# Kernel tuning notes

Hardware: AMD Instinct MI355X
Metric: run time of the kernel (lower is better)

The kernel has to match this reference:

```python
import jax, jax.numpy as jnp
import numpy as np

N = 100000
E = 3200000
C = 32

def setup_inputs() -> dict:
    key = jax.random.key(0)
    k1, k2, k3, k4 = jax.random.split(key, 4)
    adj = jax.random.uniform(k1, (E,), dtype=jnp.float32)          # per-edge weights
    labels = jax.random.uniform(k2, (N, C), dtype=jnp.float32)     # node label distributions
    src = jax.random.randint(k3, (E,), 0, N, dtype=jnp.int64)
    dst = jax.random.randint(k4, (E,), 0, N, dtype=jnp.int64)
    return {"adj": adj, "labels": labels, "src": src, "dst": dst, "n_lpa": 3}

def reference(adj, labels, src, dst, n_lpa):
    # One hop of label propagation: msg_e = label[src_e] * w_e; out_v = sum_{e: dst_e=v} msg_e
    n_nodes = labels.shape[0]

    def lp(lab):
        msg = lab[src] * adj[:, None]                 # [E, C] gather-multiply
        return jax.ops.segment_sum(msg, dst, num_segments=n_nodes)  # scatter-sum over dst

    # soft_label == 0 path of the original forward: plain iterated propagation
    for _ in range(n_lpa):
        labels = lp(labels)
    return labels
```

## Files before the change

kernel.cpp:

```cpp
#include <hip/hip_runtime.h>
#include <hip/hip_bf16.h>


#define LPA_C   32
#define BKT_LG  7
#define BKT_NV  (1 << BKT_LG)
#define CHUNK   6400

__global__ __launch_bounds__(512)
void k_histA(const int* __restrict__ dst, int* __restrict__ C,
             int E, int P, int nbkt) {
    __shared__ int h[1024];
    int c = blockIdx.x;
    int base = c * CHUNK;
    int lim = min(CHUNK, E - base);
    for (int i = threadIdx.x; i < nbkt; i += 512) h[i] = 0;
    __syncthreads();
    for (int i = threadIdx.x; i < lim; i += 512)
        atomicAdd(&h[dst[base + i] >> BKT_LG], 1);
    __syncthreads();
    for (int i = threadIdx.x; i < nbkt; i += 512) C[i * P + c] = h[i];
}

__global__ __launch_bounds__(512)
void k_scanC(int* __restrict__ C, int* __restrict__ btot, int P) {
    __shared__ int s[512];
    int b = blockIdx.x;
    int t = threadIdx.x;
    int v = (t < P) ? C[b * P + t] : 0;
    s[t] = v;
    __syncthreads();
    for (int off = 1; off < 512; off <<= 1) {
        int x = (t >= off) ? s[t - off] : 0;
        __syncthreads();
        s[t] += x;
        __syncthreads();
    }
    if (t < P) C[b * P + t] = s[t] - v;
    if (t == 511) btot[b] = s[511];
}

__global__ __launch_bounds__(1024)
void k_scanB(const int* __restrict__ btot, int* __restrict__ bstart,
             int* __restrict__ row_start, int nb, int N, int E) {
    __shared__ int s[1024];
    int t = threadIdx.x;
    int v = (t < nb) ? btot[t] : 0;
    s[t] = v;
    __syncthreads();
    for (int off = 1; off < 1024; off <<= 1) {
        int x = (t >= off) ? s[t - off] : 0;
        __syncthreads();
        s[t] += x;
        __syncthreads();
    }
    if (t < nb) bstart[t] = s[t] - v;
    if (t == 0) { bstart[nb] = E; row_start[N] = E; }
}

__global__ __launch_bounds__(512)
void k_scatA(const int* __restrict__ src, const int* __restrict__ dst,
             const float* __restrict__ adj, const int* __restrict__ C,
             const int* __restrict__ bstart, int2* __restrict__ mid,
             int E, int P, int nbkt) {
    __shared__ int2 sedge[CHUNK];
    __shared__ int  lofs[1025];
    __shared__ int  cur[1024];
    __shared__ int  s2[512];
    int c = blockIdx.x;
    int base = c * CHUNK;
    int lim = min(CHUNK, E - base);
    int t = threadIdx.x;

    for (int i = t; i < nbkt; i += 512) cur[i] = 0;
    __syncthreads();
    for (int i = t; i < lim; i += 512)
        atomicAdd(&cur[dst[base + i] >> BKT_LG], 1);
    __syncthreads();

    int k0 = 2 * t, k1 = 2 * t + 1;
    int a0 = (k0 < nbkt) ? cur[k0] : 0;
    int a1 = (k1 < nbkt) ? cur[k1] : 0;
    int ts = a0 + a1;
    s2[t] = ts;
    __syncthreads();
    for (int off = 1; off < 512; off <<= 1) {
        int x = (t >= off) ? s2[t - off] : 0;
        __syncthreads();
        s2[t] += x;
        __syncthreads();
    }
    int pre = s2[t] - ts;
    if (k0 < nbkt) lofs[k0] = pre;
    if (k1 < nbkt) lofs[k1] = pre + a0;
    if (t == 0) lofs[nbkt] = lim;
    __syncthreads();
    for (int i = t; i < nbkt; i += 512) cur[i] = lofs[i];
    __syncthreads();

    for (int i = t; i < lim; i += 512) {
        int d = dst[base + i];
        int b = d >> BKT_LG;
        int pos = atomicAdd(&cur[b], 1);
        sedge[pos] = make_int2(src[base + i] | ((d & (BKT_NV - 1)) << 20),
                               __float_as_int(adj[base + i]));
    }
    __syncthreads();

    for (int i = t; i < lim; i += 512) {
        int lo = 0, hi = nbkt;
        while (hi - lo > 1) {
            int m = (lo + hi) >> 1;
            if (lofs[m] <= i) lo = m; else hi = m;
        }
        int gdst = bstart[lo] + C[lo * P + c] + (i - lofs[lo]);
        mid[gdst] = sedge[i];
    }
}

__global__ __launch_bounds__(512)
void k_sortnode(const int2* __restrict__ mid, const int* __restrict__ bstart,
                int2* __restrict__ edges, int* __restrict__ row_start, int N) {
    __shared__ int lcnt[BKT_NV];
    __shared__ int lofs[BKT_NV];
    int b = blockIdx.x;
    int s0 = bstart[b], e0 = bstart[b + 1];
    int v0 = b << BKT_LG;
    int nv = min(BKT_NV, N - v0);

    if (threadIdx.x < BKT_NV) lcnt[threadIdx.x] = 0;
    __syncthreads();
    for (int i = s0 + threadIdx.x; i < e0; i += 512)
        atomicAdd(&lcnt[mid[i].x >> 20], 1);
    __syncthreads();
    if (threadIdx.x < BKT_NV) lofs[threadIdx.x] = lcnt[threadIdx.x];
    __syncthreads();
    for (int off = 1; off < BKT_NV; off <<= 1) {
        int x = 0;
        if (threadIdx.x < BKT_NV && threadIdx.x >= off) x = lofs[threadIdx.x - off];
        __syncthreads();
        if (threadIdx.x < BKT_NV) lofs[threadIdx.x] += x;
        __syncthreads();
    }
    if (threadIdx.x < BKT_NV) {
        int base = s0 + lofs[threadIdx.x] - lcnt[threadIdx.x];
        lcnt[threadIdx.x] = base;
        if (threadIdx.x < nv) row_start[v0 + threadIdx.x] = base;
    }
    __syncthreads();
    for (int i = s0 + threadIdx.x; i < e0; i += 512) {
        int2 ed = mid[i];
        int pos = atomicAdd(&lcnt[ed.x >> 20], 1);
        edges[pos] = make_int2(ed.x & 0xFFFFF, ed.y);
    }
}

__global__ void k_tobf16(const float* __restrict__ in, ushort* __restrict__ out, int n) {
    int i = blockIdx.x * blockDim.x + threadIdx.x;
    if (i < n) out[i] = __bfloat16_as_ushort(__float2bfloat16(in[i]));
}

template <int OUT16>
__global__ void lpa_pull16(const int2* __restrict__ edges,
                           const int* __restrict__ row_start,
                           const ushort* __restrict__ lab_in,
                           void* __restrict__ out_v, int N) {
    int node = blockIdx.x * 8 + (threadIdx.x >> 5);
    int c = threadIdx.x & 31;
    if (node >= N) return;
    int j = row_start[node];
    int end = row_start[node + 1];
    float acc0 = 0.f, acc1 = 0.f;
#define GATH(S) (__uint_as_float((unsigned)lab_in[((size_t)(unsigned)(S) << 5) + c] << 16))
    for (; j + 8 <= end; j += 8) {
        int4 q0 = *(const int4*)(edges + j);
        int4 q1 = *(const int4*)(edges + j + 2);
        int4 q2 = *(const int4*)(edges + j + 4);
        int4 q3 = *(const int4*)(edges + j + 6);
        acc0 += __int_as_float(q0.y) * GATH(q0.x);
        acc1 += __int_as_float(q0.w) * GATH(q0.z);
        acc0 += __int_as_float(q1.y) * GATH(q1.x);
        acc1 += __int_as_float(q1.w) * GATH(q1.z);
        acc0 += __int_as_float(q2.y) * GATH(q2.x);
        acc1 += __int_as_float(q2.w) * GATH(q2.z);
        acc0 += __int_as_float(q3.y) * GATH(q3.x);
        acc1 += __int_as_float(q3.w) * GATH(q3.z);
    }
    for (; j < end; ++j) {
        int2 e = edges[j];
        acc0 += __int_as_float(e.y) * GATH(e.x);
    }
#undef GATH
    float acc = acc0 + acc1;
    if (OUT16) {
        ((ushort*)out_v)[((size_t)node << 5) + c] =
            __bfloat16_as_ushort(__float2bfloat16(acc));
    } else {
        ((float*)out_v)[((size_t)node << 5) + c] = acc;
    }
}

__global__ void lpa_scatter_fb(const float* __restrict__ adj,
                               const float* __restrict__ lab_in,
                               const int* __restrict__ src,
                               const int* __restrict__ dst,
                               float* __restrict__ out, int E) {
    long long idx = (long long)blockIdx.x * blockDim.x + threadIdx.x;
    int e = (int)(idx >> 5);
    if (e >= E) return;
    int c = (int)(idx & 31);
    float v = lab_in[(long long)src[e] * LPA_C + c] * adj[e];
    unsafeAtomicAdd(&out[(long long)dst[e] * LPA_C + c], v);
}

extern "C" void kernel_launch(void* const* d_in, const int* in_sizes, int n_in,
                              void* d_out, int out_size, void* d_ws, size_t ws_size,
                              hipStream_t stream) {
    const float* adj    = (const float*)d_in[0];
    const float* labels = (const float*)d_in[1];
    const int*   src    = (const int*)d_in[2];
    const int*   dst    = (const int*)d_in[3];

    const int E  = in_sizes[0];
    const int NC = in_sizes[1];
    const int N  = NC / LPA_C;
    const int NBKT = (N + BKT_NV - 1) >> BKT_LG;
    const int P  = (E + CHUNK - 1) / CHUNK;
    float* out = (float*)d_out;

    char* p = (char*)d_ws;
    int2*  edges     = (int2*)p;  p += (size_t)E * sizeof(int2);
    int2*  mid       = (int2*)p;  p += (size_t)E * sizeof(int2);
    int*   C         = (int*)p;   p += (size_t)NBKT * P * sizeof(int);
    int*   btot      = (int*)p;   p += (size_t)NBKT * sizeof(int);
    int*   bstart    = (int*)p;   p += (size_t)(NBKT + 1) * sizeof(int);
    int*   row_start = (int*)p;   p += (size_t)(N + 1) * sizeof(int);
    size_t needed = (size_t)(p - (char*)d_ws);
    ushort* lab16_a = (ushort*)mid;
    ushort* lab16_b = (ushort*)mid + (size_t)NC;

    if (ws_size < needed || NBKT > 1024 || P > 512 || N >= (1 << 20)) {
        float* ws0 = (float*)d_ws;
        const size_t nbytes = (size_t)NC * sizeof(float);
        const long long total = (long long)E * LPA_C;
        const unsigned grid = (unsigned)((total + 255) / 256);
        hipMemsetAsync(out, 0, nbytes, stream);
        lpa_scatter_fb<<<grid, 256, 0, stream>>>(adj, labels, src, dst, out, E);
        hipMemsetAsync(ws0, 0, nbytes, stream);
        lpa_scatter_fb<<<grid, 256, 0, stream>>>(adj, out, src, dst, ws0, E);
        hipMemsetAsync(out, 0, nbytes, stream);
        lpa_scatter_fb<<<grid, 256, 0, stream>>>(adj, ws0, src, dst, out, E);
        return;
    }

    k_histA   <<<P, 512, 0, stream>>>(dst, C, E, P, NBKT);
    k_scanC   <<<NBKT, 512, 0, stream>>>(C, btot, P);
    k_scanB   <<<1, 1024, 0, stream>>>(btot, bstart, row_start, NBKT, N, E);
    k_scatA   <<<P, 512, 0, stream>>>(src, dst, adj, C, bstart, mid, E, P, NBKT);
    k_sortnode<<<NBKT, 512, 0, stream>>>(mid, bstart, edges, row_start, N);

    k_tobf16<<<(NC + 255) / 256, 256, 0, stream>>>(labels, lab16_a, NC);

    const unsigned gridN = (unsigned)((N + 7) / 8);
    lpa_pull16<1><<<gridN, 256, 0, stream>>>(edges, row_start, lab16_a, lab16_b, N);
    lpa_pull16<1><<<gridN, 256, 0, stream>>>(edges, row_start, lab16_b, lab16_a, N);
    lpa_pull16<0><<<gridN, 256, 0, stream>>>(edges, row_start, lab16_a, out, N);
}
```

Baseline: 251.0 us.

## Gather bf16 label pairs per lane and split edges across quarter-wavefronts

The pull kernel now assigns one 64-lane wavefront per node instead of 32 lanes. Each 16-lane group handles a different edge and reads two packed bf16 channels as one 32-bit word, and the groups are then combined with cross-lane shuffles. This raises the bytes per load instruction and puts more edges in flight per node, which targets the gather-bound inner loop. The cost is shuffle reductions, idle lanes on nodes with few edges, and half as many nodes per block.

```diff
diff --git a/kernel.cpp b/kernel.cpp
--- a/kernel.cpp
+++ b/kernel.cpp
@@ -161,42 +161,62 @@
 }
 
 template <int OUT16>
-__global__ void lpa_pull16(const int2* __restrict__ edges,
-                           const int* __restrict__ row_start,
-                           const ushort* __restrict__ lab_in,
-                           void* __restrict__ out_v, int N) {
-    int node = blockIdx.x * 8 + (threadIdx.x >> 5);
-    int c = threadIdx.x & 31;
+__global__ __launch_bounds__(256)
+void lpa_pull16(const int2* __restrict__ edges,
+                const int* __restrict__ row_start,
+                const ushort* __restrict__ lab_in,
+                void* __restrict__ out_v, int N) {
+    int node = blockIdx.x * 4 + (threadIdx.x >> 6);
     if (node >= N) return;
-    int j = row_start[node];
+    int lane = threadIdx.x & 63;
+    int q = lane >> 4;
+    int k = lane & 15;
+    int j   = row_start[node];
     int end = row_start[node + 1];
-    float acc0 = 0.f, acc1 = 0.f;
-#define GATH(S) (__uint_as_float((unsigned)lab_in[((size_t)(unsigned)(S) << 5) + c] << 16))
+    const unsigned* lab32 = (const unsigned*)lab_in;
+    float a00 = 0.f, a01 = 0.f, a10 = 0.f, a11 = 0.f;
     for (; j + 8 <= end; j += 8) {
-        int4 q0 = *(const int4*)(edges + j);
-        int4 q1 = *(const int4*)(edges + j + 2);
-        int4 q2 = *(const int4*)(edges + j + 4);
-        int4 q3 = *(const int4*)(edges + j + 6);
-        acc0 += __int_as_float(q0.y) * GATH(q0.x);
-        acc1 += __int_as_float(q0.w) * GATH(q0.z);
-        acc0 += __int_as_float(q1.y) * GATH(q1.x);
-        acc1 += __int_as_float(q1.w) * GATH(q1.z);
-        acc0 += __int_as_float(q2.y) * GATH(q2.x);
-        acc1 += __int_as_float(q2.w) * GATH(q2.z);
-        acc0 += __int_as_float(q3.y) * GATH(q3.x);
-        acc1 += __int_as_float(q3.w) * GATH(q3.z);
-    }
-    for (; j < end; ++j) {
-        int2 e = edges[j];
-        acc0 += __int_as_float(e.y) * GATH(e.x);
-    }
-#undef GATH
-    float acc = acc0 + acc1;
-    if (OUT16) {
-        ((ushort*)out_v)[((size_t)node << 5) + c] =
-            __bfloat16_as_ushort(__float2bfloat16(acc));
-    } else {
-        ((float*)out_v)[((size_t)node << 5) + c] = acc;
+        int2 e0 = edges[j + q];
+        int2 e1 = edges[j + 4 + q];
+        unsigned v0 = lab32[((size_t)(unsigned)e0.x << 4) + k];
+        unsigned v1 = lab32[((size_t)(unsigned)e1.x << 4) + k];
+        float w0 = __int_as_float(e0.y);
+        float w1 = __int_as_float(e1.y);
+        a00 += w0 * __uint_as_float(v0 << 16);
+        a01 += w0 * __uint_as_float(v0 & 0xFFFF0000u);
+        a10 += w1 * __uint_as_float(v1 << 16);
+        a11 += w1 * __uint_as_float(v1 & 0xFFFF0000u);
+    }
+    if (j + 4 <= end) {
+        int2 e0 = edges[j + q];
+        unsigned v0 = lab32[((size_t)(unsigned)e0.x << 4) + k];
+        float w0 = __int_as_float(e0.y);
+        a00 += w0 * __uint_as_float(v0 << 16);
+        a01 += w0 * __uint_as_float(v0 & 0xFFFF0000u);
+        j += 4;
+    }
+    if (j < end && q < end - j) {
+        int2 e0 = edges[j + q];
+        unsigned v0 = lab32[((size_t)(unsigned)e0.x << 4) + k];
+        float w0 = __int_as_float(e0.y);
+        a00 += w0 * __uint_as_float(v0 << 16);
+        a01 += w0 * __uint_as_float(v0 & 0xFFFF0000u);
+    }
+    float a0 = a00 + a10;
+    float a1 = a01 + a11;
+    a0 += __shfl_xor(a0, 16);
+    a0 += __shfl_xor(a0, 32);
+    a1 += __shfl_xor(a1, 16);
+    a1 += __shfl_xor(a1, 32);
+    if (q == 0) {
+        if (OUT16) {
+            unsigned pk = (((unsigned)__bfloat16_as_ushort(__float2bfloat16(a1))) << 16)
+                        |  ((unsigned)__bfloat16_as_ushort(__float2bfloat16(a0)));
+            ((unsigned*)out_v)[((size_t)node << 4) + k] = pk;
+        } else {
+            float2 f2 = make_float2(a0, a1);
+            ((float2*)out_v)[((size_t)node << 4) + k] = f2;
+        }
     }
 }
 
@@ -261,7 +281,7 @@
 
     k_tobf16<<<(NC + 255) / 256, 256, 0, stream>>>(labels, lab16_a, NC);
 
-    const unsigned gridN = (unsigned)((N + 7) / 8);
+    const unsigned gridN = (unsigned)((N + 3) / 4);
     lpa_pull16<1><<<gridN, 256, 0, stream>>>(edges, row_start, lab16_a, lab16_b, N);
     lpa_pull16<1><<<gridN, 256, 0, stream>>>(edges, row_start, lab16_b, lab16_a, N);
     lpa_pull16<0><<<gridN, 256, 0, stream>>>(edges, row_start, lab16_a, out, N);
```

New measurement: 258.2 us. 2.9% more time.

## Split label channels into two 16-wide halves and propagate each separately

Applied to the files above, without the earlier changes.

Labels are stored as two separate 16-channel bf16 arrays, and all three propagation hops run independently for each half, so the gathered working set per pass is halved. The pull kernel now assigns a 64-lane wave per node, with four edges processed concurrently across lane groups, multiple accumulators and a shuffle reduction. The cost is reading the CSR edge list twice and launching twice as many propagation kernels.

```diff
diff --git a/kernel.cpp b/kernel.cpp
--- a/kernel.cpp
+++ b/kernel.cpp
@@ -155,48 +155,68 @@
     }
 }
 
-__global__ void k_tobf16(const float* __restrict__ in, ushort* __restrict__ out, int n) {
+__global__ void k_tobf16s(const float* __restrict__ in, ushort* __restrict__ lo,
+                          ushort* __restrict__ hi, int NC) {
     int i = blockIdx.x * blockDim.x + threadIdx.x;
-    if (i < n) out[i] = __bfloat16_as_ushort(__float2bfloat16(in[i]));
+    if (i >= NC) return;
+    int n = i >> 5, c = i & 31;
+    ushort v = __bfloat16_as_ushort(__float2bfloat16(in[i]));
+    if (c < 16) lo[((size_t)n << 4) + c] = v;
+    else        hi[((size_t)n << 4) + (c - 16)] = v;
 }
 
 template <int OUT16>
-__global__ void lpa_pull16(const int2* __restrict__ edges,
-                           const int* __restrict__ row_start,
-                           const ushort* __restrict__ lab_in,
-                           void* __restrict__ out_v, int N) {
-    int node = blockIdx.x * 8 + (threadIdx.x >> 5);
-    int c = threadIdx.x & 31;
+__global__ __launch_bounds__(256)
+void lpa_pull8(const int2* __restrict__ edges,
+               const int* __restrict__ row_start,
+               const ushort* __restrict__ lab_in,
+               void* __restrict__ out_v, int N) {
+    int node = blockIdx.x * 4 + (threadIdx.x >> 6);
     if (node >= N) return;
-    int j = row_start[node];
-    int end = row_start[node + 1];
-    float acc0 = 0.f, acc1 = 0.f;
-#define GATH(S) (__uint_as_float((unsigned)lab_in[((size_t)(unsigned)(S) << 5) + c] << 16))
-    for (; j + 8 <= end; j += 8) {
-        int4 q0 = *(const int4*)(edges + j);
-        int4 q1 = *(const int4*)(edges + j + 2);
-        int4 q2 = *(const int4*)(edges + j + 4);
-        int4 q3 = *(const int4*)(edges + j + 6);
-        acc0 += __int_as_float(q0.y) * GATH(q0.x);
-        acc1 += __int_as_float(q0.w) * GATH(q0.z);
-        acc0 += __int_as_float(q1.y) * GATH(q1.x);
-        acc1 += __int_as_float(q1.w) * GATH(q1.z);
-        acc0 += __int_as_float(q2.y) * GATH(q2.x);
-        acc1 += __int_as_float(q2.w) * GATH(q2.z);
-        acc0 += __int_as_float(q3.y) * GATH(q3.x);
-        acc1 += __int_as_float(q3.w) * GATH(q3.z);
-    }
-    for (; j < end; ++j) {
-        int2 e = edges[j];
-        acc0 += __int_as_float(e.y) * GATH(e.x);
-    }
-#undef GATH
-    float acc = acc0 + acc1;
-    if (OUT16) {
-        ((ushort*)out_v)[((size_t)node << 5) + c] =
-            __bfloat16_as_ushort(__float2bfloat16(acc));
-    } else {
-        ((float*)out_v)[((size_t)node << 5) + c] = acc;
+    int lane = threadIdx.x & 63;
+    int h = (lane >> 5) & 1;
+    int s = (lane >> 4) & 1;
+    int c = lane & 15;
+    int eslot = 2 * h + s;
+    int j   = __builtin_amdgcn_readfirstlane(row_start[node]);
+    int end = __builtin_amdgcn_readfirstlane(row_start[node + 1]);
+    float a0 = 0.f, a1 = 0.f, a2 = 0.f, a3 = 0.f;
+#define GRP(J, ACC) {                                                          \
+        int4 q0 = *(const int4*)(edges + (J));                                 \
+        int4 q1 = *(const int4*)(edges + (J) + 2);                             \
+        int sx = h ? q1.x : q0.x;  int sz = h ? q1.z : q0.z;                   \
+        int wy = h ? q1.y : q0.y;  int ww = h ? q1.w : q0.w;                   \
+        int srcv = s ? sz : sx;    int wv = s ? ww : wy;                       \
+        ACC += __int_as_float(wv) *                                            \
+               __uint_as_float((unsigned)lab_in[((size_t)(unsigned)srcv << 4) + c] << 16); }
+    for (; j + 16 <= end; j += 16) {
+        GRP(j, a0)
+        GRP(j + 4, a1)
+        GRP(j + 8, a2)
+        GRP(j + 12, a3)
+    }
+    for (; j + 4 <= end; j += 4) {
+        GRP(j, a0)
+    }
+    if (j < end) {
+        int rem = end - j;
+        if (eslot < rem) {
+            int2 r = edges[j + eslot];
+            a0 += __int_as_float(r.y) *
+                  __uint_as_float((unsigned)lab_in[((size_t)(unsigned)r.x << 4) + c] << 16);
+        }
+    }
+#undef GRP
+    float acc = (a0 + a1) + (a2 + a3);
+    acc += __shfl_xor(acc, 16);
+    acc += __shfl_xor(acc, 32);
+    if (lane < 16) {
+        if (OUT16) {
+            ((ushort*)out_v)[((size_t)node << 4) + c] =
+                __bfloat16_as_ushort(__float2bfloat16(acc));
+        } else {
+            ((float*)out_v)[((size_t)node << 5) + c] = acc;
+        }
     }
 }
 
@@ -236,8 +256,10 @@
     int*   bstart    = (int*)p;   p += (size_t)(NBKT + 1) * sizeof(int);
     int*   row_start = (int*)p;   p += (size_t)(N + 1) * sizeof(int);
     size_t needed = (size_t)(p - (char*)d_ws);
-    ushort* lab16_a = (ushort*)mid;
-    ushort* lab16_b = (ushort*)mid + (size_t)NC;
+    ushort* lo_a = (ushort*)mid;
+    ushort* lo_b = lo_a + (size_t)N * 16;
+    ushort* hi_a = lo_b + (size_t)N * 16;
+    ushort* hi_b = hi_a + (size_t)N * 16;
 
     if (ws_size < needed || NBKT > 1024 || P > 512 || N >= (1 << 20)) {
         float* ws0 = (float*)d_ws;
@@ -259,10 +281,15 @@
     k_scatA   <<<P, 512, 0, stream>>>(src, dst, adj, C, bstart, mid, E, P, NBKT);
     k_sortnode<<<NBKT, 512, 0, stream>>>(mid, bstart, edges, row_start, N);
 
-    k_tobf16<<<(NC + 255) / 256, 256, 0, stream>>>(labels, lab16_a, NC);
-
-    const unsigned gridN = (unsigned)((N + 7) / 8);
-    lpa_pull16<1><<<gridN, 256, 0, stream>>>(edges, row_start, lab16_a, lab16_b, N);
-    lpa_pull16<1><<<gridN, 256, 0, stream>>>(edges, row_start, lab16_b, lab16_a, N);
-    lpa_pull16<0><<<gridN, 256, 0, stream>>>(edges, row_start, lab16_a, out, N);
-}
+    k_tobf16s<<<(NC + 255) / 256, 256, 0, stream>>>(labels, lo_a, hi_a, NC);
+
+    const unsigned gridN = (unsigned)((N + 3) / 4);
+
+    lpa_pull8<1><<<gridN, 256, 0, stream>>>(edges, row_start, lo_a, lo_b, N);
+    lpa_pull8<1><<<gridN, 256, 0, stream>>>(edges, row_start, lo_b, lo_a, N);
+    lpa_pull8<0><<<gridN, 256, 0, stream>>>(edges, row_start, lo_a, out, N);
+
+    lpa_pull8<1><<<gridN, 256, 0, stream>>>(edges, row_start, hi_a, hi_b, N);
+    lpa_pull8<1><<<gridN, 256, 0, stream>>>(edges, row_start, hi_b, hi_a, N);
+    lpa_pull8<0><<<gridN, 256, 0, stream>>>(edges, row_start, hi_a, out + 16, N);
+}
```

After: 329.0 us. 31.1% more time.
